# Kernel tuning notes

Hardware: AMD Instinct MI355X
Metric: run time of the kernel (lower is better)

The kernel has to match this reference:

```python
import jax, jax.numpy as jnp
import numpy as np

N = 25000
E = 400000
F = 8            # scalar node features (irreps_in = 8x0e)
NB = 8           # num bessel radial basis
R_MAX = 4.0      # edge_cutoff
MLPSZ = 64
S0, V0 = 64, 32  # hidden: 64x0e + 32x1o
MS, MV = F + S0, V0          # conv input mults after skip-concat: 72 scalars, 32 vectors
NW0 = 2 * F                  # layer-0 tp weights per edge (s*sh0->0, s*sh1->1)
NW = 2 * MS + 3 * MV         # deeper layers: 240 tp weights per edge
MOUT_S = MS + MV             # 104 scalar message channels
MOUT_V = MS + 2 * MV         # 136 vector message channels
SQRT3, SQRT2 = 3.0 ** 0.5, 2.0 ** 0.5
INV_SQRT_DEG = (E / N) ** -0.5  # 1/sqrt(avg degree 16)


def _radial(r):
    # Bessel basis with polynomial cutoff envelope (MACE RadialEmbeddingBlock)
    n = jnp.arange(1, NB + 1, dtype=r.dtype)
    bess = jnp.sqrt(2.0 / R_MAX) * jnp.sin(n * jnp.pi * r / R_MAX) / r  # [E, NB]
    x = jnp.clip(r / R_MAX, 0.0, 1.0)
    p = 6.0
    env = 1.0 - 0.5 * (p + 1) * (p + 2) * x ** p + p * (p + 2) * x ** (p + 1) - 0.5 * p * (p + 1) * x ** (p + 2)
    env = env * (x < 1.0)
    return bess * env


def _mlp(r_emb, w1, b1, w2, b2):
    return jax.nn.silu(r_emb @ w1 + b1) @ w2 + b2


def _forward(x_feat, edge_vec, mlp0_w1, mlp0_b1, mlp0_w2, mlp0_b2, lin0_ws, lin0_wv,
             mlp1_w1, mlp1_b1, mlp1_w2, mlp1_b2, lin1_ws, lin1_wv,
             mlp2_w1, mlp2_b1, mlp2_w2, mlp2_b2, lin2_ws, lin2_wv,
             ro_w, ro_b, ptype, edge_index):
    seg = jax.ops.segment_sum
    src, dst = edge_index[0], edge_index[1]
    r = jnp.linalg.norm(edge_vec, axis=1, keepdims=True)          # [E,1]
    sh1 = SQRT3 * edge_vec / r                                    # l=1 SH ('component' norm); sh0 == 1
    r_emb = _radial(r)                                            # [E,NB]

    node_in = x_feat                                              # NodeEmbedding: scalar features
    node_copy = jax.lax.stop_gradient(node_in)                    # skip_conn uses detached copy

    # --- layer 0: input = F scalars only ---
    w = _mlp(r_emb, mlp0_w1, mlp0_b1, mlp0_w2, mlp0_b2)           # [E, 2F]
    w_ss, w_sv = w[:, :F], w[:, F:]
    s_e = node_in[src]                                            # [E,F]
    agg_s = seg(s_e * w_ss, dst, num_segments=N) * INV_SQRT_DEG   # [N,F]
    m_v = s_e[:, :, None] * sh1[:, None, :] * w_sv[:, :, None]    # [E,F,3]
    agg_v = seg(m_v, dst, num_segments=N) * INV_SQRT_DEG          # [N,F,3]
    s = jax.nn.silu(agg_s @ lin0_ws)                              # [N,S0]
    v = jnp.einsum('nmd,mo->nod', agg_v, lin0_wv)                 # [N,V0,3]

    # --- layers 1..2 (residual, equal irreps) ---
    for (w1, b1, w2, b2, ls, lv) in ((mlp1_w1, mlp1_b1, mlp1_w2, mlp1_b2, lin1_ws, lin1_wv),
                                     (mlp2_w1, mlp2_b1, mlp2_w2, mlp2_b2, lin2_ws, lin2_wv)):
        s_in = jnp.concatenate([node_copy, s], axis=-1)           # [N,MS]
        w = _mlp(r_emb, w1, b1, w2, b2)                           # [E,NW]
        w_ss = w[:, :MS]
        w_vs = w[:, MS:MS + MV]
        w_sv = w[:, MS + MV:2 * MS + MV]
        w_v0 = w[:, 2 * MS + MV:2 * MS + 2 * MV]
        w_v1 = w[:, 2 * MS + 2 * MV:]
        s_e, v_e = s_in[src], v[src]                              # [E,MS], [E,MV,3]
        dot = jnp.sum(v_e * sh1[:, None, :], axis=-1) / SQRT3     # 1o x 1o -> 0e
        m_s = jnp.concatenate([s_e * w_ss, dot * w_vs], axis=-1)  # [E,MOUT_S]
        m_v = jnp.concatenate([
            s_e[:, :, None] * sh1[:, None, :] * w_sv[:, :, None],           # 0e x 1o -> 1o
            v_e * w_v0[:, :, None],                                         # 1o x 0e -> 1o
            (jnp.cross(v_e, sh1[:, None, :]) / SQRT2) * w_v1[:, :, None],   # 1o x 1o -> 1o
        ], axis=1)                                                # [E,MOUT_V,3]
        agg_s = seg(m_s, dst, num_segments=N) * INV_SQRT_DEG
        agg_v = seg(m_v, dst, num_segments=N) * INV_SQRT_DEG
        s = s + jax.nn.silu(agg_s @ ls)
        v = v + jnp.einsum('nmd,mo->nod', agg_v, lv)

    # readout: scalars + vector norms, per-particle-type linear
    vnorm = jnp.sqrt(jnp.sum(v * v, axis=-1) + 1e-12)             # [N,V0]
    feats = jnp.concatenate([s, vnorm], axis=-1)                  # [N,S0+V0]
    return jnp.einsum('nd,ndo->no', feats, ro_w[ptype]) + ro_b[ptype]


def setup_inputs() -> dict:
    key = jax.random.key(0)
    ks = jax.random.split(key, 20)
    lin = lambda k, shp, fan: jax.random.normal(k, shp, jnp.float32) / np.sqrt(fan).astype(np.float32)
    d = {}
    d['x_feat'] = jax.random.normal(ks[0], (N, F), jnp.float32)
    d['ptype'] = jax.random.randint(ks[1], (N,), 0, 2, jnp.int32)
    d['edge_index'] = jax.random.randint(ks[2], (2, E), 0, N, jnp.int32)
    d['edge_vec'] = jax.random.normal(ks[3], (E, 3), jnp.float32)
    d['mlp0_w1'] = lin(ks[4], (NB, MLPSZ), NB); d['mlp0_b1'] = jnp.zeros((MLPSZ,), jnp.float32)
    d['mlp0_w2'] = lin(ks[5], (MLPSZ, NW0), MLPSZ); d['mlp0_b2'] = jnp.zeros((NW0,), jnp.float32)
    d['lin0_ws'] = lin(ks[6], (F, S0), F); d['lin0_wv'] = lin(ks[7], (F, V0), F)
    d['mlp1_w1'] = lin(ks[8], (NB, MLPSZ), NB); d['mlp1_b1'] = jnp.zeros((MLPSZ,), jnp.float32)
    d['mlp1_w2'] = lin(ks[9], (MLPSZ, NW), MLPSZ); d['mlp1_b2'] = jnp.zeros((NW,), jnp.float32)
    d['lin1_ws'] = lin(ks[10], (MOUT_S, S0), MOUT_S); d['lin1_wv'] = lin(ks[11], (MOUT_V, V0), MOUT_V)
    d['mlp2_w1'] = lin(ks[12], (NB, MLPSZ), NB); d['mlp2_b1'] = jnp.zeros((MLPSZ,), jnp.float32)
    d['mlp2_w2'] = lin(ks[13], (MLPSZ, NW), MLPSZ); d['mlp2_b2'] = jnp.zeros((NW,), jnp.float32)
    d['lin2_ws'] = lin(ks[14], (MOUT_S, S0), MOUT_S); d['lin2_wv'] = lin(ks[15], (MOUT_V, V0), MOUT_V)
    d['ro_w'] = lin(ks[16], (2, S0 + V0, 10), S0 + V0); d['ro_b'] = jnp.zeros((2, 10), jnp.float32)
    return d


def reference(x_feat, ptype, edge_index, edge_vec, mlp0_w1, mlp0_b1, mlp0_w2, mlp0_b2, lin0_ws, lin0_wv,
              mlp1_w1, mlp1_b1, mlp1_w2, mlp1_b2, lin1_ws, lin1_wv,
              mlp2_w1, mlp2_b1, mlp2_w2, mlp2_b2, lin2_ws, lin2_wv, ro_w, ro_b):
    return _forward(x_feat, edge_vec, mlp0_w1, mlp0_b1, mlp0_w2, mlp0_b2, lin0_ws, lin0_wv,
                    mlp1_w1, mlp1_b1, mlp1_w2, mlp1_b2, lin1_ws, lin1_wv,
                    mlp2_w1, mlp2_b1, mlp2_w2, mlp2_b2, lin2_ws, lin2_wv,
                    ro_w, ro_b, ptype, edge_index)
```

## Files before the change

### kernel.cpp

```cpp
#include <hip/hip_runtime.h>
#include <math.h>

#define N_NODES 25000
#define N_EDGES 400000
#define IDEG 0.25f
#define SQRT3F 1.7320508075688772f
#define INV_SQRT3F 0.5773502691896258f
#define INV_SQRT2F 0.7071067811865476f
#define SCAN_NBLK 25

__device__ __forceinline__ float silu_f(float x) {
  return x / (1.0f + __expf(-x));
}

__global__ __launch_bounds__(256) void edge_pre_k(
    const int* __restrict__ ei, const float* __restrict__ evec,
    float* __restrict__ remb, float* __restrict__ sh1, int* __restrict__ deg) {
  int e = blockIdx.x * 256 + threadIdx.x;
  if (e >= N_EDGES) return;
  float x = evec[3*e+0], y = evec[3*e+1], z = evec[3*e+2];
  float r = sqrtf(x*x + y*y + z*z);
  float inv_r = 1.0f / r;
  sh1[3*e+0] = SQRT3F * x * inv_r;
  sh1[3*e+1] = SQRT3F * y * inv_r;
  sh1[3*e+2] = SQRT3F * z * inv_r;
  float xr = r * 0.25f;
  float xc = fminf(xr, 1.0f);
  float xc2 = xc*xc, xc3 = xc2*xc, xc6 = xc3*xc3, xc7 = xc6*xc, xc8 = xc7*xc;
  float env = 1.0f - 28.0f*xc6 + 48.0f*xc7 - 21.0f*xc8;
  env = (xr < 1.0f) ? env : 0.0f;
  float coef = 0.7071067811865476f * env * inv_r;
  float wv = 0.7853981633974483f * r;
  float s1 = sinf(wv), c1 = cosf(wv);
  float twoc = 2.0f * c1;
  float sp = 0.0f, sc = s1;
  #pragma unroll
  for (int n = 1; n <= 8; ++n) {
    remb[e*8 + n - 1] = coef * sc;
    float sn = twoc * sc - sp;
    sp = sc; sc = sn;
  }
  atomicAdd(&deg[ei[N_EDGES + e]], 1);
}

__global__ __launch_bounds__(1024) void scanA_k(
    const int* __restrict__ deg, int* __restrict__ rp, int* __restrict__ part) {
  __shared__ int sm[1024];
  int tid = threadIdx.x;
  int idx = blockIdx.x * 1024 + tid;
  int v = (idx < N_NODES) ? deg[idx] : 0;
  sm[tid] = v;
  __syncthreads();
  for (int off = 1; off < 1024; off <<= 1) {
    int t = (tid >= off) ? sm[tid - off] : 0;
    __syncthreads();
    sm[tid] += t;
    __syncthreads();
  }
  if (idx < N_NODES) rp[idx + 1] = sm[tid];
  if (tid == 1023) part[blockIdx.x] = sm[1023];
}

__global__ void scanB_k(int* __restrict__ part) {
  if (threadIdx.x == 0) {
    int acc = 0;
    for (int b = 0; b < SCAN_NBLK; ++b) { int t = part[b]; part[b] = acc; acc += t; }
  }
}

__global__ __launch_bounds__(1024) void scanC_k(
    const int* __restrict__ deg, int* __restrict__ rp, int* __restrict__ cursor,
    const int* __restrict__ part) {
  int idx = blockIdx.x * 1024 + threadIdx.x;
  if (idx >= N_NODES) return;
  int incl = rp[idx + 1] + part[blockIdx.x];
  rp[idx + 1] = incl;
  cursor[idx] = incl - deg[idx];
  if (idx == 0) rp[0] = 0;
}

__global__ __launch_bounds__(256) void scatter_k(
    const int* __restrict__ ei, int* __restrict__ cursor, int* __restrict__ seid) {
  int e = blockIdx.x * 256 + threadIdx.x;
  if (e >= N_EDGES) return;
  int d = ei[N_EDGES + e];
  int pos = atomicAdd(&cursor[d], 1);
  seid[pos] = e;
}

__global__ __launch_bounds__(64) void layer0_k(
    const int* __restrict__ ei, const int* __restrict__ rp, const int* __restrict__ seid,
    const float* __restrict__ remb, const float* __restrict__ sh1,
    const float* __restrict__ xfeat,
    const float* __restrict__ w1, const float* __restrict__ b1,
    const float* __restrict__ w2, const float* __restrict__ b2,
    const float* __restrict__ ws0, const float* __restrict__ wv0,
    float* __restrict__ sinb, float* __restrict__ vb) {
  int n = blockIdx.x;
  int lane = threadIdx.x;
  __shared__ float w1_l[512];
  __shared__ float w2_l[1024];
  __shared__ float h_l[64];
  __shared__ float w_l[16];
  __shared__ float agg_l[32];
  for (int i = lane; i < 512; i += 64) w1_l[i] = w1[i];
  for (int i = lane; i < 1024; i += 64) w2_l[i] = w2[i];
  float b1r = b1[lane];
  int p0 = rp[n], p1 = rp[n+1];
  float acc = 0.0f;
  for (int p = p0; p < p1; ++p) {
    int e = seid[p];
    int src = ei[e];
    float re[8];
    #pragma unroll
    for (int q = 0; q < 8; ++q) re[q] = remb[e*8+q];
    float sx = sh1[3*e], sy = sh1[3*e+1], sz = sh1[3*e+2];
    __syncthreads();
    float ha = b1r;
    #pragma unroll
    for (int q = 0; q < 8; ++q) ha += re[q] * w1_l[q*64 + lane];
    h_l[lane] = silu_f(ha);
    __syncthreads();
    if (lane < 16) {
      float wa = b2[lane];
      for (int k = 0; k < 64; ++k) wa += h_l[k] * w2_l[k*16 + lane];
      w_l[lane] = wa;
    }
    __syncthreads();
    if (lane < 8) {
      acc += xfeat[src*8 + lane] * w_l[lane];
    } else if (lane < 32) {
      int c = lane - 8;
      int i = c / 3, d = c - 3*(c/3);
      float sh = (d == 0) ? sx : ((d == 1) ? sy : sz);
      acc += xfeat[src*8 + i] * sh * w_l[8 + i];
    }
  }
  __syncthreads();
  if (lane < 32) agg_l[lane] = acc * IDEG;
  __syncthreads();
  float so = 0.0f;
  #pragma unroll
  for (int m = 0; m < 8; ++m) so += agg_l[m] * ws0[m*64 + lane];
  sinb[n*72 + 8 + lane] = silu_f(so);
  if (lane < 8) sinb[n*72 + lane] = xfeat[n*8 + lane];
  for (int pr = lane; pr < 96; pr += 64) {
    int o = pr / 3, d = pr - 3*(pr/3);
    float va = 0.0f;
    #pragma unroll
    for (int m = 0; m < 8; ++m) va += agg_l[8 + m*3 + d] * wv0[m*32 + o];
    vb[n*96 + pr] = va;
  }
}

__global__ __launch_bounds__(256, 2) void mlp_big_k(
    const int* __restrict__ rp, const int* __restrict__ seid,
    const float* __restrict__ remb,
    const float* __restrict__ w1, const float* __restrict__ b1,
    const float* __restrict__ w2, const float* __restrict__ b2,
    float* __restrict__ wbuf, int nlo, int nhi) {
  __shared__ float w2_l[64*240];
  __shared__ float h_l[64*65];
  __shared__ float re_l[64*9];
  __shared__ int   eid_l[64];
  int tid = threadIdx.x;
  int plo = rp[nlo], phi = rp[nhi];
  int tp0 = plo + blockIdx.x * 64;
  if (tp0 >= phi) return;
  for (int i = tid*4; i < 15360; i += 1024)
    *(float4*)&w2_l[i] = *(const float4*)&w2[i];
  if (tid < 64) {
    int p = tp0 + tid;
    eid_l[tid] = seid[p < phi ? p : (phi - 1)];
  }
  __syncthreads();
  {
    int eg = tid >> 2, q2 = (tid & 3) * 2;
    int e = eid_l[eg];
    re_l[eg*9 + q2]     = remb[e*8 + q2];
    re_l[eg*9 + q2 + 1] = remb[e*8 + q2 + 1];
  }
  __syncthreads();
  {
    int eg = tid & 63, kb = (tid >> 6) * 16;
    for (int k = kb; k < kb + 16; ++k) {
      float a = b1[k];
      #pragma unroll
      for (int q = 0; q < 8; ++q) a += re_l[eg*9 + q] * w1[q*64 + k];
      h_l[eg*65 + k] = silu_f(a);
    }
  }
  __syncthreads();
  int lane = tid & 63, j0 = (tid >> 6) * 60;
  float c[60];
  #pragma unroll
  for (int j = 0; j < 60; ++j) c[j] = b2[j0 + j];
  for (int k = 0; k < 64; ++k) {
    float a = h_l[lane*65 + k];
    #pragma unroll
    for (int jj = 0; jj < 15; ++jj) {
      float4 b = *(const float4*)&w2_l[k*240 + j0 + jj*4];
      c[jj*4+0] += a * b.x; c[jj*4+1] += a * b.y;
      c[jj*4+2] += a * b.z; c[jj*4+3] += a * b.w;
    }
  }
  float* outp = wbuf + (size_t)(tp0 - plo + lane) * 240 + j0;
  #pragma unroll
  for (int jj = 0; jj < 15; ++jj)
    *(float4*)&outp[jj*4] = make_float4(c[jj*4], c[jj*4+1], c[jj*4+2], c[jj*4+3]);
}

__global__ __launch_bounds__(64) void gather_k(
    const int* __restrict__ ei, const int* __restrict__ rp, const int* __restrict__ seid,
    const float* __restrict__ sh1, const float* __restrict__ wbuf,
    const float* __restrict__ sin_prev, const float* __restrict__ v_prev,
    const float* __restrict__ xfeat,
    const float* __restrict__ ls, const float* __restrict__ lv,
    float* __restrict__ sin_out, float* __restrict__ v_out, int nlo) {
  int n = nlo + blockIdx.x;
  int lane = threadIdx.x;
  __shared__ float w_l[240];
  __shared__ float se_l[72];
  __shared__ float ve_l[96];
  __shared__ float agg_l[512];
  int p0 = rp[n], p1 = rp[n+1];
  int plo = rp[nlo];
  float acc0=0,acc1=0,acc2=0,acc3=0,acc4=0,acc5=0,acc6=0,acc7=0;
  for (int p = p0; p < p1; ++p) {
    int e = seid[p];
    int src = ei[e];
    const float* wrow = wbuf + (size_t)(p - plo) * 240;
    float sx = sh1[3*e], sy = sh1[3*e+1], sz = sh1[3*e+2];
    __syncthreads();
    w_l[lane]      = wrow[lane];
    w_l[64+lane]   = wrow[64+lane];
    w_l[128+lane]  = wrow[128+lane];
    if (lane < 48) w_l[192+lane] = wrow[192+lane];
    se_l[lane] = sin_prev[(size_t)src*72 + lane];
    if (lane < 8)  se_l[64+lane] = sin_prev[(size_t)src*72 + 64 + lane];
    ve_l[lane] = v_prev[(size_t)src*96 + lane];
    if (lane < 32) ve_l[64+lane] = v_prev[(size_t)src*96 + 64 + lane];
    __syncthreads();
    acc0 += se_l[lane] * w_l[lane];
    {
      int f = 64 + lane;
      float m;
      if (f < 72) m = se_l[f] * w_l[f];
      else if (f < 104) {
        int i = f - 72;
        float dot = (ve_l[i*3]*sx + ve_l[i*3+1]*sy + ve_l[i*3+2]*sz) * INV_SQRT3F;
        m = dot * w_l[72 + i];
      } else {
        int cc = f - 104; int j = cc/3, d = cc - 3*(cc/3);
        float sh = (d==0) ? sx : ((d==1) ? sy : sz);
        m = se_l[j] * sh * w_l[104 + j];
      }
      acc1 += m;
    }
    #pragma unroll
    for (int t = 2; t <= 4; ++t) {
      int cc = 64*t + lane - 104;
      int j = cc/3, d = cc - 3*(cc/3);
      float sh = (d==0) ? sx : ((d==1) ? sy : sz);
      float m = se_l[j] * sh * w_l[104 + j];
      if (t == 2) acc2 += m; else if (t == 3) acc3 += m; else acc4 += m;
    }
    acc5 += ve_l[lane] * w_l[176 + lane/3];
    {
      if (lane < 32) {
        int cc = 64 + lane;
        acc6 += ve_l[cc] * w_l[176 + cc/3];
      } else {
        int cc = lane - 32; int i = cc/3, d = cc - 3*(cc/3);
        float a0 = ve_l[i*3], a1 = ve_l[i*3+1], a2 = ve_l[i*3+2];
        float cr = (d==0) ? (a1*sz - a2*sy) : ((d==1) ? (a2*sx - a0*sz) : (a0*sy - a1*sx));
        acc6 += cr * INV_SQRT2F * w_l[208 + i];
      }
    }
    {
      int cc = 32 + lane; int i = cc/3, d = cc - 3*(cc/3);
      float a0 = ve_l[i*3], a1 = ve_l[i*3+1], a2 = ve_l[i*3+2];
      float cr = (d==0) ? (a1*sz - a2*sy) : ((d==1) ? (a2*sx - a0*sz) : (a0*sy - a1*sx));
      acc7 += cr * INV_SQRT2F * w_l[208 + i];
    }
  }
  __syncthreads();
  agg_l[lane]       = acc0 * IDEG;
  agg_l[64 + lane]  = acc1 * IDEG;
  agg_l[128 + lane] = acc2 * IDEG;
  agg_l[192 + lane] = acc3 * IDEG;
  agg_l[256 + lane] = acc4 * IDEG;
  agg_l[320 + lane] = acc5 * IDEG;
  agg_l[384 + lane] = acc6 * IDEG;
  agg_l[448 + lane] = acc7 * IDEG;
  __syncthreads();
  float so = 0.0f;
  for (int m = 0; m < 104; ++m) so += agg_l[m] * ls[m*64 + lane];
  sin_out[(size_t)n*72 + 8 + lane] = sin_prev[(size_t)n*72 + 8 + lane] + silu_f(so);
  if (lane < 8) sin_out[(size_t)n*72 + lane] = xfeat[n*8 + lane];
  for (int pr = lane; pr < 96; pr += 64) {
    int o = pr / 3, d = pr - 3*(pr/3);
    float va = 0.0f;
    for (int m = 0; m < 136; ++m) va += agg_l[104 + m*3 + d] * lv[m*32 + o];
    v_out[(size_t)n*96 + pr] = v_prev[(size_t)n*96 + pr] + va;
  }
}

__global__ __launch_bounds__(64) void readout_k(
    const float* __restrict__ sinb, const float* __restrict__ vb,
    const int* __restrict__ ptype, const float* __restrict__ row,
    const float* __restrict__ rob, float* __restrict__ out) {
  int n = blockIdx.x;
  int lane = threadIdx.x;
  __shared__ float f_l[96];
  f_l[lane] = sinb[(size_t)n*72 + 8 + lane];
  if (lane < 32) {
    float a = vb[(size_t)n*96 + lane*3];
    float b = vb[(size_t)n*96 + lane*3 + 1];
    float c = vb[(size_t)n*96 + lane*3 + 2];
    f_l[64 + lane] = sqrtf(a*a + b*b + c*c + 1e-12f);
  }
  __syncthreads();
  if (lane < 10) {
    int pt = ptype[n];
    const float* wr = row + pt * 960;
    float acc = rob[pt*10 + lane];
    for (int j = 0; j < 96; ++j) acc += f_l[j] * wr[j*10 + lane];
    out[n*10 + lane] = acc;
  }
}

extern "C" void kernel_launch(void* const* d_in, const int* in_sizes, int n_in,
                              void* d_out, int out_size, void* d_ws, size_t ws_size,
                              hipStream_t stream) {
  (void)in_sizes; (void)n_in; (void)out_size;
  const float* xfeat = (const float*)d_in[0];
  const int*   ptype = (const int*)d_in[1];
  const int*   ei    = (const int*)d_in[2];
  const float* evec  = (const float*)d_in[3];
  const float* m0w1  = (const float*)d_in[4];
  const float* m0b1  = (const float*)d_in[5];
  const float* m0w2  = (const float*)d_in[6];
  const float* m0b2  = (const float*)d_in[7];
  const float* l0ws  = (const float*)d_in[8];
  const float* l0wv  = (const float*)d_in[9];
  const float* mw1[2] = {(const float*)d_in[10], (const float*)d_in[16]};
  const float* mb1[2] = {(const float*)d_in[11], (const float*)d_in[17]};
  const float* mw2[2] = {(const float*)d_in[12], (const float*)d_in[18]};
  const float* mb2[2] = {(const float*)d_in[13], (const float*)d_in[19]};
  const float* lws[2] = {(const float*)d_in[14], (const float*)d_in[20]};
  const float* lwv[2] = {(const float*)d_in[15], (const float*)d_in[21]};
  const float* row   = (const float*)d_in[22];
  const float* rob   = (const float*)d_in[23];
  float* out = (float*)d_out;

  float* ws   = (float*)d_ws;
  float* remb = ws;
  float* sh1  = remb + (size_t)N_EDGES*8;
  float* sin0 = sh1  + (size_t)N_EDGES*3;
  float* sin1 = sin0 + (size_t)N_NODES*72;
  float* v0   = sin1 + (size_t)N_NODES*72;
  float* v1   = v0   + (size_t)N_NODES*96;
  int* deg    = (int*)(v1 + (size_t)N_NODES*96);
  int* rp     = deg + N_NODES;
  int* cursor = rp + N_NODES + 1;
  int* part   = cursor + N_NODES;
  int* seid   = part + 32;
  float* wbuf = (float*)(seid + N_EDGES + 3);

  size_t fixed = (size_t)(wbuf - ws);
  size_t avail = (ws_size / 4 > fixed) ? (ws_size / 4 - fixed) : 0;
  int NC = 1;
  while (NC < 1024 && (size_t)(N_EDGES / NC + 8256) * 240 > avail) NC <<= 1;
  int cap = N_EDGES / NC + 8192;

  hipMemsetAsync(deg, 0, N_NODES * sizeof(int), stream);
  edge_pre_k<<<(N_EDGES + 255) / 256, 256, 0, stream>>>(ei, evec, remb, sh1, deg);
  scanA_k<<<SCAN_NBLK, 1024, 0, stream>>>(deg, rp, part);
  scanB_k<<<1, 64, 0, stream>>>(part);
  scanC_k<<<SCAN_NBLK, 1024, 0, stream>>>(deg, rp, cursor, part);
  scatter_k<<<(N_EDGES + 255) / 256, 256, 0, stream>>>(ei, cursor, seid);
  layer0_k<<<N_NODES, 64, 0, stream>>>(ei, rp, seid, remb, sh1, xfeat,
      m0w1, m0b1, m0w2, m0b2, l0ws, l0wv, sin0, v0);

  const float* sin_in = sin0; const float* v_in = v0;
  float* sin_out = sin1; float* v_out = v1;
  for (int l = 0; l < 2; ++l) {
    for (int c = 0; c < NC; ++c) {
      int nlo = (int)((long long)N_NODES * c / NC);
      int nhi = (int)((long long)N_NODES * (c + 1) / NC);
      mlp_big_k<<<(cap + 63) / 64, 256, 0, stream>>>(rp, seid, remb,
          mw1[l], mb1[l], mw2[l], mb2[l], wbuf, nlo, nhi);
      gather_k<<<nhi - nlo, 64, 0, stream>>>(ei, rp, seid, sh1, wbuf,
          sin_in, v_in, xfeat, lws[l], lwv[l], sin_out, v_out, nlo);
    }
    const float* t;
    t = sin_in; sin_in = sin_out; sin_out = (float*)t;
    t = v_in;   v_in = v_out;     v_out = (float*)t;
  }
  readout_k<<<N_NODES, 64, 0, stream>>>(sin_in, v_in, ptype, row, rob, out);
}
```

Baseline: 1.584 ms.

## Fuse layer-0 edge MLP into edge prep with atomics, prefetch gather, drop LDS w2

Layer-0 radial MLP and message computation now run per edge inside the edge preprocessing kernel, scattering results into a per-node aggregate with float atomics. A small finish kernel applies the node linear layers, replacing the per-node serial edge loop and its many barriers. The deeper-layer MLP kernel now reads w2 from global memory (scalar-uniform addressing) instead of staging 60KB in LDS. The gather kernel software-prefetches the next edge's data into registers. Float atomics make layer-0 summation order nondeterministic and add atomic traffic.

```diff
diff --git a/kernel.cpp b/kernel.cpp
--- a/kernel.cpp
+++ b/kernel.cpp
@@ -15,15 +15,18 @@
 
 __global__ __launch_bounds__(256) void edge_pre_k(
     const int* __restrict__ ei, const float* __restrict__ evec,
-    float* __restrict__ remb, float* __restrict__ sh1, int* __restrict__ deg) {
+    const float* __restrict__ xfeat,
+    const float* __restrict__ w1, const float* __restrict__ b1,
+    const float* __restrict__ w2, const float* __restrict__ b2,
+    float* __restrict__ remb, float* __restrict__ sh1,
+    int* __restrict__ deg, float* __restrict__ agg0) {
   int e = blockIdx.x * 256 + threadIdx.x;
   if (e >= N_EDGES) return;
   float x = evec[3*e+0], y = evec[3*e+1], z = evec[3*e+2];
   float r = sqrtf(x*x + y*y + z*z);
   float inv_r = 1.0f / r;
-  sh1[3*e+0] = SQRT3F * x * inv_r;
-  sh1[3*e+1] = SQRT3F * y * inv_r;
-  sh1[3*e+2] = SQRT3F * z * inv_r;
+  float sx = SQRT3F * x * inv_r, sy = SQRT3F * y * inv_r, sz = SQRT3F * z * inv_r;
+  sh1[3*e+0] = sx; sh1[3*e+1] = sy; sh1[3*e+2] = sz;
   float xr = r * 0.25f;
   float xc = fminf(xr, 1.0f);
   float xc2 = xc*xc, xc3 = xc2*xc, xc6 = xc3*xc3, xc7 = xc6*xc, xc8 = xc7*xc;
@@ -34,13 +37,65 @@
   float s1 = sinf(wv), c1 = cosf(wv);
   float twoc = 2.0f * c1;
   float sp = 0.0f, sc = s1;
+  float re[8];
   #pragma unroll
   for (int n = 1; n <= 8; ++n) {
-    remb[e*8 + n - 1] = coef * sc;
+    re[n-1] = coef * sc;
     float sn = twoc * sc - sp;
     sp = sc; sc = sn;
   }
-  atomicAdd(&deg[ei[N_EDGES + e]], 1);
+  *(float4*)&remb[(size_t)e*8]     = make_float4(re[0], re[1], re[2], re[3]);
+  *(float4*)&remb[(size_t)e*8 + 4] = make_float4(re[4], re[5], re[6], re[7]);
+  int src = ei[e], dst = ei[N_EDGES + e];
+  atomicAdd(&deg[dst], 1);
+  float w0a[16];
+  #pragma unroll
+  for (int j = 0; j < 16; ++j) w0a[j] = b2[j];
+  #pragma unroll
+  for (int k = 0; k < 64; ++k) {
+    float a = b1[k];
+    #pragma unroll
+    for (int q = 0; q < 8; ++q) a += re[q] * w1[q*64 + k];
+    float hk = silu_f(a);
+    #pragma unroll
+    for (int j = 0; j < 16; ++j) w0a[j] += hk * w2[k*16 + j];
+  }
+  float4 xa = ((const float4*)(xfeat + (size_t)src*8))[0];
+  float4 xb = ((const float4*)(xfeat + (size_t)src*8))[1];
+  float se[8] = {xa.x, xa.y, xa.z, xa.w, xb.x, xb.y, xb.z, xb.w};
+  float* base = agg0 + (size_t)dst * 32;
+  #pragma unroll
+  for (int i = 0; i < 8; ++i) atomicAdd(base + i, se[i] * w0a[i]);
+  #pragma unroll
+  for (int i = 0; i < 8; ++i) {
+    float t = se[i] * w0a[8 + i];
+    atomicAdd(base + 8 + i*3 + 0, t * sx);
+    atomicAdd(base + 8 + i*3 + 1, t * sy);
+    atomicAdd(base + 8 + i*3 + 2, t * sz);
+  }
+}
+
+__global__ __launch_bounds__(64) void layer0_finish_k(
+    const float* __restrict__ agg0, const float* __restrict__ xfeat,
+    const float* __restrict__ ws0, const float* __restrict__ wv0,
+    float* __restrict__ sinb, float* __restrict__ vb) {
+  int n = blockIdx.x;
+  int lane = threadIdx.x;
+  __shared__ float agg_l[32];
+  if (lane < 32) agg_l[lane] = agg0[(size_t)n*32 + lane] * IDEG;
+  __syncthreads();
+  float so = 0.0f;
+  #pragma unroll
+  for (int m = 0; m < 8; ++m) so += agg_l[m] * ws0[m*64 + lane];
+  sinb[(size_t)n*72 + 8 + lane] = silu_f(so);
+  if (lane < 8) sinb[(size_t)n*72 + lane] = xfeat[n*8 + lane];
+  for (int pr = lane; pr < 96; pr += 64) {
+    int o = pr / 3, d = pr - 3*(pr/3);
+    float va = 0.0f;
+    #pragma unroll
+    for (int m = 0; m < 8; ++m) va += agg_l[8 + m*3 + d] * wv0[m*32 + o];
+    vb[(size_t)n*96 + pr] = va;
+  }
 }
 
 __global__ __launch_bounds__(1024) void scanA_k(
@@ -88,78 +143,12 @@
   seid[pos] = e;
 }
 
-__global__ __launch_bounds__(64) void layer0_k(
-    const int* __restrict__ ei, const int* __restrict__ rp, const int* __restrict__ seid,
-    const float* __restrict__ remb, const float* __restrict__ sh1,
-    const float* __restrict__ xfeat,
-    const float* __restrict__ w1, const float* __restrict__ b1,
-    const float* __restrict__ w2, const float* __restrict__ b2,
-    const float* __restrict__ ws0, const float* __restrict__ wv0,
-    float* __restrict__ sinb, float* __restrict__ vb) {
-  int n = blockIdx.x;
-  int lane = threadIdx.x;
-  __shared__ float w1_l[512];
-  __shared__ float w2_l[1024];
-  __shared__ float h_l[64];
-  __shared__ float w_l[16];
-  __shared__ float agg_l[32];
-  for (int i = lane; i < 512; i += 64) w1_l[i] = w1[i];
-  for (int i = lane; i < 1024; i += 64) w2_l[i] = w2[i];
-  float b1r = b1[lane];
-  int p0 = rp[n], p1 = rp[n+1];
-  float acc = 0.0f;
-  for (int p = p0; p < p1; ++p) {
-    int e = seid[p];
-    int src = ei[e];
-    float re[8];
-    #pragma unroll
-    for (int q = 0; q < 8; ++q) re[q] = remb[e*8+q];
-    float sx = sh1[3*e], sy = sh1[3*e+1], sz = sh1[3*e+2];
-    __syncthreads();
-    float ha = b1r;
-    #pragma unroll
-    for (int q = 0; q < 8; ++q) ha += re[q] * w1_l[q*64 + lane];
-    h_l[lane] = silu_f(ha);
-    __syncthreads();
-    if (lane < 16) {
-      float wa = b2[lane];
-      for (int k = 0; k < 64; ++k) wa += h_l[k] * w2_l[k*16 + lane];
-      w_l[lane] = wa;
-    }
-    __syncthreads();
-    if (lane < 8) {
-      acc += xfeat[src*8 + lane] * w_l[lane];
-    } else if (lane < 32) {
-      int c = lane - 8;
-      int i = c / 3, d = c - 3*(c/3);
-      float sh = (d == 0) ? sx : ((d == 1) ? sy : sz);
-      acc += xfeat[src*8 + i] * sh * w_l[8 + i];
-    }
-  }
-  __syncthreads();
-  if (lane < 32) agg_l[lane] = acc * IDEG;
-  __syncthreads();
-  float so = 0.0f;
-  #pragma unroll
-  for (int m = 0; m < 8; ++m) so += agg_l[m] * ws0[m*64 + lane];
-  sinb[n*72 + 8 + lane] = silu_f(so);
-  if (lane < 8) sinb[n*72 + lane] = xfeat[n*8 + lane];
-  for (int pr = lane; pr < 96; pr += 64) {
-    int o = pr / 3, d = pr - 3*(pr/3);
-    float va = 0.0f;
-    #pragma unroll
-    for (int m = 0; m < 8; ++m) va += agg_l[8 + m*3 + d] * wv0[m*32 + o];
-    vb[n*96 + pr] = va;
-  }
-}
-
-__global__ __launch_bounds__(256, 2) void mlp_big_k(
+__global__ __launch_bounds__(256) void mlp_big_k(
     const int* __restrict__ rp, const int* __restrict__ seid,
     const float* __restrict__ remb,
     const float* __restrict__ w1, const float* __restrict__ b1,
     const float* __restrict__ w2, const float* __restrict__ b2,
     float* __restrict__ wbuf, int nlo, int nhi) {
-  __shared__ float w2_l[64*240];
   __shared__ float h_l[64*65];
   __shared__ float re_l[64*9];
   __shared__ int   eid_l[64];
@@ -167,8 +156,6 @@
   int plo = rp[nlo], phi = rp[nhi];
   int tp0 = plo + blockIdx.x * 64;
   if (tp0 >= phi) return;
-  for (int i = tid*4; i < 15360; i += 1024)
-    *(float4*)&w2_l[i] = *(const float4*)&w2[i];
   if (tid < 64) {
     int p = tp0 + tid;
     eid_l[tid] = seid[p < phi ? p : (phi - 1)];
@@ -191,15 +178,18 @@
     }
   }
   __syncthreads();
-  int lane = tid & 63, j0 = (tid >> 6) * 60;
+  int lane = tid & 63;
+  int j0 = __builtin_amdgcn_readfirstlane(((int)threadIdx.x >> 6) * 60);
   float c[60];
   #pragma unroll
   for (int j = 0; j < 60; ++j) c[j] = b2[j0 + j];
+  const float* hrow = &h_l[lane*65];
   for (int k = 0; k < 64; ++k) {
-    float a = h_l[lane*65 + k];
+    float a = hrow[k];
+    const float* w2r = w2 + k*240 + j0;
     #pragma unroll
     for (int jj = 0; jj < 15; ++jj) {
-      float4 b = *(const float4*)&w2_l[k*240 + j0 + jj*4];
+      float4 b = *(const float4*)&w2r[jj*4];
       c[jj*4+0] += a * b.x; c[jj*4+1] += a * b.y;
       c[jj*4+2] += a * b.z; c[jj*4+3] += a * b.w;
     }
@@ -226,20 +216,40 @@
   int p0 = rp[n], p1 = rp[n+1];
   int plo = rp[nlo];
   float acc0=0,acc1=0,acc2=0,acc3=0,acc4=0,acc5=0,acc6=0,acc7=0;
+  float nw0=0,nw1=0,nw2=0,nw3=0,nse0=0,nse1=0,nve0=0,nve1=0,nsx=0,nsy=0,nsz=0;
+  if (p0 < p1) {
+    int e = seid[p0]; int src = ei[e];
+    const float* wr = wbuf + (size_t)(p0 - plo) * 240;
+    nsx = sh1[3*e]; nsy = sh1[3*e+1]; nsz = sh1[3*e+2];
+    nw0 = wr[lane]; nw1 = wr[64+lane]; nw2 = wr[128+lane];
+    if (lane < 48) nw3 = wr[192+lane];
+    nse0 = sin_prev[(size_t)src*72 + lane];
+    if (lane < 8)  nse1 = sin_prev[(size_t)src*72 + 64 + lane];
+    nve0 = v_prev[(size_t)src*96 + lane];
+    if (lane < 32) nve1 = v_prev[(size_t)src*96 + 64 + lane];
+  }
   for (int p = p0; p < p1; ++p) {
-    int e = seid[p];
-    int src = ei[e];
-    const float* wrow = wbuf + (size_t)(p - plo) * 240;
-    float sx = sh1[3*e], sy = sh1[3*e+1], sz = sh1[3*e+2];
+    float sx = nsx, sy = nsy, sz = nsz;
     __syncthreads();
-    w_l[lane]      = wrow[lane];
-    w_l[64+lane]   = wrow[64+lane];
-    w_l[128+lane]  = wrow[128+lane];
-    if (lane < 48) w_l[192+lane] = wrow[192+lane];
-    se_l[lane] = sin_prev[(size_t)src*72 + lane];
-    if (lane < 8)  se_l[64+lane] = sin_prev[(size_t)src*72 + 64 + lane];
-    ve_l[lane] = v_prev[(size_t)src*96 + lane];
-    if (lane < 32) ve_l[64+lane] = v_prev[(size_t)src*96 + 64 + lane];
+    w_l[lane]      = nw0;
+    w_l[64+lane]   = nw1;
+    w_l[128+lane]  = nw2;
+    if (lane < 48) w_l[192+lane] = nw3;
+    se_l[lane] = nse0;
+    if (lane < 8)  se_l[64+lane] = nse1;
+    ve_l[lane] = nve0;
+    if (lane < 32) ve_l[64+lane] = nve1;
+    if (p + 1 < p1) {
+      int e = seid[p+1]; int src = ei[e];
+      const float* wr = wbuf + (size_t)(p+1 - plo) * 240;
+      nsx = sh1[3*e]; nsy = sh1[3*e+1]; nsz = sh1[3*e+2];
+      nw0 = wr[lane]; nw1 = wr[64+lane]; nw2 = wr[128+lane];
+      if (lane < 48) nw3 = wr[192+lane];
+      nse0 = sin_prev[(size_t)src*72 + lane];
+      if (lane < 8)  nse1 = sin_prev[(size_t)src*72 + 64 + lane];
+      nve0 = v_prev[(size_t)src*96 + lane];
+      if (lane < 32) nve1 = v_prev[(size_t)src*96 + 64 + lane];
+    }
     __syncthreads();
     acc0 += se_l[lane] * w_l[lane];
     {
@@ -361,7 +371,8 @@
   float* sin1 = sin0 + (size_t)N_NODES*72;
   float* v0   = sin1 + (size_t)N_NODES*72;
   float* v1   = v0   + (size_t)N_NODES*96;
-  int* deg    = (int*)(v1 + (size_t)N_NODES*96);
+  float* agg0 = v1   + (size_t)N_NODES*96;
+  int* deg    = (int*)(agg0 + (size_t)N_NODES*32);
   int* rp     = deg + N_NODES;
   int* cursor = rp + N_NODES + 1;
   int* part   = cursor + N_NODES;
@@ -375,13 +386,14 @@
   int cap = N_EDGES / NC + 8192;
 
   hipMemsetAsync(deg, 0, N_NODES * sizeof(int), stream);
-  edge_pre_k<<<(N_EDGES + 255) / 256, 256, 0, stream>>>(ei, evec, remb, sh1, deg);
+  hipMemsetAsync(agg0, 0, (size_t)N_NODES * 32 * sizeof(float), stream);
+  edge_pre_k<<<(N_EDGES + 255) / 256, 256, 0, stream>>>(ei, evec, xfeat,
+      m0w1, m0b1, m0w2, m0b2, remb, sh1, deg, agg0);
   scanA_k<<<SCAN_NBLK, 1024, 0, stream>>>(deg, rp, part);
   scanB_k<<<1, 64, 0, stream>>>(part);
   scanC_k<<<SCAN_NBLK, 1024, 0, stream>>>(deg, rp, cursor, part);
   scatter_k<<<(N_EDGES + 255) / 256, 256, 0, stream>>>(ei, cursor, seid);
-  layer0_k<<<N_NODES, 64, 0, stream>>>(ei, rp, seid, remb, sh1, xfeat,
-      m0w1, m0b1, m0w2, m0b2, l0ws, l0wv, sin0, v0);
+  layer0_finish_k<<<N_NODES, 64, 0, stream>>>(agg0, xfeat, l0ws, l0wv, sin0, v0);
 
   const float* sin_in = sin0; const float* v_in = v0;
   float* sin_out = sin1; float* v_out = v1;
```

After: 1.808 ms. 1.14x slower.
